# Performance work log

Measured on AMD Instinct MI355X. Metric: run time of the kernel, lower is better.

The kernel has to match this reference:

```python
import jax, jax.numpy as jnp
import numpy as np

N = 2          # batch (upsample scale for sample i is i+1, shapes chosen so no crop occurs)
C = 512        # channels for both branches
TH = TW = 256  # target H,W taken from pts_feats[0]
IMG_SIZES = [128, 64, 32, 16, 8]  # 5-level FPN
BN_EPS = 1e-5


def setup_inputs() -> dict:
    key = jax.random.key(0)
    ks = jax.random.split(key, 24)
    inp = {}
    for l, s in enumerate(IMG_SIZES):
        inp[f'img_feat{l}'] = jax.random.normal(ks[l], (N, C, s, s), jnp.float32)
    inp['pts_feat0'] = jax.random.normal(ks[5], (N, C, TH, TW), jnp.float32)
    # 1x1 conv + BN params (eval-mode BN with running stats)
    inp['img_w'] = jax.random.normal(ks[6], (C, C), jnp.float32) * 0.02
    inp['img_b'] = jax.random.normal(ks[7], (C,), jnp.float32) * 0.02
    inp['img_gamma'] = jnp.ones((C,), jnp.float32)
    inp['img_beta'] = jnp.zeros((C,), jnp.float32)
    inp['img_mean'] = jnp.zeros((C,), jnp.float32)
    inp['img_var'] = jax.random.uniform(ks[8], (C,), jnp.float32, 0.5, 1.5)
    inp['pts_w'] = jax.random.normal(ks[9], (C, C), jnp.float32) * 0.02
    inp['pts_b'] = jax.random.normal(ks[10], (C,), jnp.float32) * 0.02
    inp['pts_gamma'] = jnp.ones((C,), jnp.float32)
    inp['pts_beta'] = jnp.zeros((C,), jnp.float32)
    inp['pts_mean'] = jnp.zeros((C,), jnp.float32)
    inp['pts_var'] = jax.random.uniform(ks[11], (C,), jnp.float32, 0.5, 1.5)
    return inp


def _obtain_mlvl(feats, th, tw):
    # Faithful to original: per-sample loop (scale_factor depends on batch index,
    # so each sample has a different static upsampled shape -> Python loop over N=2).
    n = feats[0].shape[0]
    outs = []
    for i in range(n):
        acc = None
        for lvl, f in enumerate(feats):
            x = f[i]  # [C, h, w]
            if lvl > 0:
                s = i + 1  # nearest upsample by batch-index+1 (as in source)
                x = jnp.repeat(jnp.repeat(x, s, axis=1), s, axis=2)
            dh = th - x.shape[1]
            dw = tw - x.shape[2]
            x = jnp.pad(x, ((0, 0), (dh // 2, dh - dh // 2), (dw // 2, dw - dw // 2)), mode='edge')
            acc = x if acc is None else acc + x
        outs.append(acc)
    return jnp.stack(outs, 0)  # [N, C, th, tw]


def _conv_bn_relu(x, w, b, gamma, beta, mean, var):
    # 1x1 conv == channel contraction, then eval-mode BN, then ReLU
    y = jnp.einsum('nchw,oc->nohw', x, w) + b[None, :, None, None]
    scale = gamma / jnp.sqrt(var + BN_EPS)
    y = (y - mean[None, :, None, None]) * scale[None, :, None, None] + beta[None, :, None, None]
    return jax.nn.relu(y)


def reference(img_feat0, img_feat1, img_feat2, img_feat3, img_feat4, pts_feat0,
              img_w, img_b, img_gamma, img_beta, img_mean, img_var,
              pts_w, pts_b, pts_gamma, pts_beta, pts_mean, pts_var):
    th, tw = pts_feat0.shape[2], pts_feat0.shape[3]
    pts_m = _obtain_mlvl([pts_feat0], th, tw)  # pts_levels=1
    pts_pre = _conv_bn_relu(pts_m, pts_w, pts_b, pts_gamma, pts_beta, pts_mean, pts_var)
    img_m = _obtain_mlvl([img_feat0, img_feat1, img_feat2, img_feat3, img_feat4], th, tw)
    img_pre = _conv_bn_relu(img_m, img_w, img_b, img_gamma, img_beta, img_mean, img_var)
    # dropout is identity in eval mode (deterministic reference)
    return jnp.concatenate((img_pre, pts_pre), axis=1)  # [N, 2C, th, tw]
```

## Files before the change

kernel.cpp:

```cpp
#include <hip/hip_runtime.h>

typedef unsigned short u16;
typedef __attribute__((ext_vector_type(8))) short s8frag;
typedef __attribute__((ext_vector_type(4))) float f32x4;

#define GLOAD16(gp, lp)                                                        \
  __builtin_amdgcn_global_load_lds(                                            \
      (const __attribute__((address_space(1))) void*)(gp),                     \
      (__attribute__((address_space(3))) void*)(lp), 16, 0, 0)

__device__ __forceinline__ u16 f2bf(float x) {
  unsigned int u = __float_as_uint(x);
  unsigned int r = (u + 0x7fffu + ((u >> 16) & 1u)) >> 16;
  return (u16)r;
}

__global__ __launch_bounds__(256) void build_b(
    const float* __restrict__ f0, const float* __restrict__ f1,
    const float* __restrict__ f2, const float* __restrict__ f3,
    const float* __restrict__ f4, const float* __restrict__ pts,
    const float* __restrict__ wi, const float* __restrict__ bi,
    const float* __restrict__ gi, const float* __restrict__ bei,
    const float* __restrict__ mi, const float* __restrict__ vi,
    const float* __restrict__ wp, const float* __restrict__ bp,
    const float* __restrict__ gp, const float* __restrict__ bep,
    const float* __restrict__ mp, const float* __restrict__ vp,
    u16* __restrict__ Bimg, u16* __restrict__ Bpts,
    u16* __restrict__ wA_img, float* __restrict__ bias_i,
    u16* __restrict__ wA_pts, float* __restrict__ bias_p) {
  int t = threadIdx.x;
  int z = blockIdx.z;

  if (z == 32) {
    int base = ((blockIdx.y * 4 + blockIdx.x) * 256 + t) * 2;
#pragma unroll
    for (int e = 0; e < 2; ++e) {
      int gidx = base + e;
      int branch = gidx >> 18;
      int idx = gidx & ((1 << 18) - 1);
      int o = idx >> 9, c = idx & 511;
      const float* w = branch ? wp : wi;
      const float* b = branch ? bp : bi;
      const float* g = branch ? gp : gi;
      const float* be = branch ? bep : bei;
      const float* mn = branch ? mp : mi;
      const float* vr = branch ? vp : vi;
      u16* wo = branch ? wA_pts : wA_img;
      float* bo = branch ? bias_p : bias_i;
      float scale = g[o] * rsqrtf(vr[o] + 1e-5f);
      wo[idx] = f2bf(w[idx] * scale);
      if (c == 0) bo[o] = scale * (b[o] - mn[o]) + be[o];
    }
    return;
  }

  int wblk = blockIdx.x;
  int h = blockIdx.y;
  bool is_img = z < 16;
  int zz = is_img ? z : z - 16;
  int n = zz >> 3;
  int cblk = zz & 7;
  int cbase = cblk * 64;

  if (is_img) {
    __shared__ u16 btile[64][8][8];
    int wl = t & 63, w = wblk * 64 + wl;
    int cg = t >> 6;
    const float* feats[5] = {f0, f1, f2, f3, f4};
    const int S[5] = {128, 64, 32, 16, 8};
    long gbase[5];
#pragma unroll
    for (int l = 0; l < 5; ++l) {
      int sl = S[l];
      int sh = (n == 1 && l > 0) ? 1 : 0;
      int u = sl << sh, pad = (256 - u) >> 1;
      int ih = h - pad; ih = ih < 0 ? 0 : (ih > u - 1 ? u - 1 : ih); ih >>= sh;
      int iw = w - pad; iw = iw < 0 ? 0 : (iw > u - 1 ? u - 1 : iw); iw >>= sh;
      gbase[l] = (long)(n * 512) * sl * sl + ih * sl + iw;
    }
#pragma unroll
    for (int it = 0; it < 2; ++it) {
      int chunk = cg + it * 4;
      int c0 = cbase + chunk * 8;
      u16 pk[8];
#pragma unroll
      for (int j = 0; j < 8; ++j) {
        int c = c0 + j;
        float a_ = 0.f;
#pragma unroll
        for (int l = 0; l < 5; ++l)
          a_ += feats[l][gbase[l] + (long)c * (S[l] * S[l])];
        pk[j] = f2bf(a_);
      }
      *(uint4*)&btile[wl][chunk ^ (wl & 7)][0] = *(const uint4*)pk;
    }
    __syncthreads();
#pragma unroll
    for (int half = 0; half < 2; ++half) {
      int w2 = half * 32 + (t >> 3);
      int kcl = t & 7;
      uint4 v = *(const uint4*)&btile[w2][kcl ^ (w2 & 7)][0];
      long di = ((long)n * 65536 + (long)h * 256 + wblk * 64 + w2) * 512 +
                cbase + kcl * 8;
      *(uint4*)(Bimg + di) = v;
    }
    return;
  }

  __shared__ float tile[64][65];
  int wq = t & 15;
  int cl0 = t >> 4;
#pragma unroll
  for (int j = 0; j < 4; ++j) {
    int cl = cl0 + j * 16;
    int c = cbase + cl;
    float4 v = *(const float4*)&pts[((long)(n * 512 + c) * 256 + h) * 256 +
                                    wblk * 64 + wq * 4];
    tile[cl][wq * 4 + 0] = v.x;
    tile[cl][wq * 4 + 1] = v.y;
    tile[cl][wq * 4 + 2] = v.z;
    tile[cl][wq * 4 + 3] = v.w;
  }
  __syncthreads();

  long hwb = (long)h * 256 + wblk * 64;
#pragma unroll
  for (int half = 0; half < 2; ++half) {
    int c0 = (t & 7) * 8;
    int wl2 = half * 32 + (t >> 3);
    u16 p[8];
#pragma unroll
    for (int j = 0; j < 8; ++j) p[j] = f2bf(tile[c0 + j][wl2]);
    long di = ((long)n * 65536 + hwb + wl2) * 512 + cbase + c0;
    *(uint4*)(Bpts + di) = *(const uint4*)p;
  }
}

__global__ __launch_bounds__(1024, 1) void gemm_fused(
    const u16* __restrict__ Aimg, const u16* __restrict__ Apts,
    const u16* __restrict__ Bimg, const u16* __restrict__ Bpts,
    const float* __restrict__ biasImg, const float* __restrict__ biasPts,
    float* __restrict__ out) {
  int br = blockIdx.z;
  const u16* A = br ? Apts : Aimg;
  const u16* B = br ? Bpts : Bimg;
  const float* bias = br ? biasPts : biasImg;

  int s = blockIdx.x;
  int w = (s & 7) * 128 + (s >> 3);
  int rt = w & 1;
  int ct = w >> 1;
  int n = ct >> 8;
  int colbase = (ct & 255) * 256;
  const u16* Bn = B + ((long)n * 65536) * 512;

  __shared__ u16 As[3][256 * 32];
  __shared__ u16 Bs[3][256 * 32];

  int t = threadIdx.x;
  int wave = t >> 6, lane = t & 63;
  int wr = wave >> 2, wc = wave & 3;
  int lrow = lane & 15;
  int q = lane >> 4;

  f32x4 acc[4][4] = {};

#define STAGE(buf, kt_)                                                       \
  {                                                                           \
    int kk_ = (kt_) * 32;                                                     \
    int row = t >> 2, kp = t & 3;                                             \
    int sw = (row >> 1) & 3;                                                  \
    GLOAD16(A + ((long)(rt * 256 + row) * 512 + kk_ + ((kp ^ sw) * 8)),       \
            &As[buf][(t) * 8]);                                               \
    GLOAD16(Bn + ((long)(colbase + row) * 512 + kk_ + ((kp ^ sw) * 8)),       \
            &Bs[buf][(t) * 8]);                                               \
  }

  STAGE(0, 0);
  STAGE(1, 1);
  asm volatile("s_waitcnt vmcnt(2)" ::: "memory");
  __builtin_amdgcn_s_barrier();

#pragma unroll 1
  for (int kt = 0; kt < 16; ++kt) {
    int cur = kt % 3;
    s8frag a[4], b[4];
#pragma unroll
    for (int m = 0; m < 4; ++m) {
      int r = wr * 64 + m * 16 + lrow;
      a[m] = *(const s8frag*)&As[cur][r * 32 + ((q ^ ((r >> 1) & 3)) * 8)];
    }
#pragma unroll
    for (int nn = 0; nn < 4; ++nn) {
      int r = wc * 64 + nn * 16 + lrow;
      b[nn] = *(const s8frag*)&Bs[cur][r * 32 + ((q ^ ((r >> 1) & 3)) * 8)];
    }
    if (kt < 14) STAGE((kt + 2) % 3, kt + 2);
    __builtin_amdgcn_s_setprio(1);
#pragma unroll
    for (int m = 0; m < 4; ++m)
#pragma unroll
      for (int nn = 0; nn < 4; ++nn)
        acc[m][nn] =
            __builtin_amdgcn_mfma_f32_16x16x32_bf16(b[nn], a[m], acc[m][nn], 0, 0, 0);
    __builtin_amdgcn_s_setprio(0);
    if (kt < 15) {
      if (kt < 14)
        asm volatile("s_waitcnt vmcnt(2)" ::: "memory");
      else
        asm volatile("s_waitcnt vmcnt(0)" ::: "memory");
      __builtin_amdgcn_s_barrier();
    }
  }
#undef STAGE

  long outbase = ((long)n * 1024 + br * 512) * 65536;
#pragma unroll
  for (int m = 0; m < 4; ++m) {
    int o = rt * 256 + wr * 64 + m * 16 + lrow;
    float bv = bias[o];
    long orow = outbase + (long)o * 65536;
#pragma unroll
    for (int nn = 0; nn < 4; ++nn) {
      int hwq = colbase + wc * 64 + nn * 16 + q * 4;
      f32x4 v;
#pragma unroll
      for (int j = 0; j < 4; ++j) {
        float x = acc[m][nn][j] + bv;
        v[j] = x > 0.f ? x : 0.f;
      }
      *(f32x4*)(out + orow + hwq) = v;
    }
  }
}

extern "C" void kernel_launch(void* const* d_in, const int* in_sizes, int n_in,
                              void* d_out, int out_size, void* d_ws,
                              size_t ws_size, hipStream_t stream) {
  (void)in_sizes; (void)n_in; (void)out_size; (void)ws_size;
  const float* f0 = (const float*)d_in[0];
  const float* f1 = (const float*)d_in[1];
  const float* f2 = (const float*)d_in[2];
  const float* f3 = (const float*)d_in[3];
  const float* f4 = (const float*)d_in[4];
  const float* pts = (const float*)d_in[5];
  const float* img_w = (const float*)d_in[6];
  const float* img_b = (const float*)d_in[7];
  const float* img_gamma = (const float*)d_in[8];
  const float* img_beta = (const float*)d_in[9];
  const float* img_mean = (const float*)d_in[10];
  const float* img_var = (const float*)d_in[11];
  const float* pts_w = (const float*)d_in[12];
  const float* pts_b = (const float*)d_in[13];
  const float* pts_gamma = (const float*)d_in[14];
  const float* pts_beta = (const float*)d_in[15];
  const float* pts_mean = (const float*)d_in[16];
  const float* pts_var = (const float*)d_in[17];

  char* ws = (char*)d_ws;
  u16* wA_img = (u16*)ws;
  u16* wA_pts = wA_img + 512 * 512;
  float* bias_img = (float*)(ws + (1u << 20));
  float* bias_pts = bias_img + 512;
  u16* Bimg = (u16*)(ws + (2u << 20));
  u16* Bpts = Bimg + (size_t)2 * 65536 * 512;

  build_b<<<dim3(4, 256, 33), 256, 0, stream>>>(
      f0, f1, f2, f3, f4, pts, img_w, img_b, img_gamma, img_beta, img_mean,
      img_var, pts_w, pts_b, pts_gamma, pts_beta, pts_mean, pts_var, Bimg,
      Bpts, wA_img, bias_img, wA_pts, bias_pts);
  gemm_fused<<<dim3(1024, 1, 2), 1024, 0, stream>>>(
      wA_img, wA_pts, Bimg, Bpts, bias_img, bias_pts, (float*)d_out);
}
```

Baseline: 406.3 us.

## Make GEMM persistent over 8 column tiles with continuous cross-tile prefetch

```diff
diff --git a/kernel.cpp b/kernel.cpp
--- a/kernel.cpp
+++ b/kernel.cpp
@@ -146,13 +146,15 @@
   const u16* B = br ? Bpts : Bimg;
   const float* bias = br ? biasPts : biasImg;
 
-  int s = blockIdx.x;
-  int w = (s & 7) * 128 + (s >> 3);
+  int s0 = blockIdx.x;
+  int w = (s0 & 7) * 16 + (s0 >> 3);
   int rt = w & 1;
-  int ct = w >> 1;
-  int n = ct >> 8;
-  int colbase = (ct & 255) * 256;
+  int grp = w >> 1;
+  int ct0 = grp * 8;
+  int n = ct0 >> 8;
+  int colbase0 = (ct0 & 255) * 256;
   const u16* Bn = B + ((long)n * 65536) * 512;
+  long outbase = ((long)n * 1024 + br * 512) * 65536;
 
   __shared__ u16 As[3][256 * 32];
   __shared__ u16 Bs[3][256 * 32];
@@ -165,25 +167,26 @@
 
   f32x4 acc[4][4] = {};
 
-#define STAGE(buf, kt_)                                                       \
+#define STAGE(s_)                                                             \
   {                                                                           \
-    int kk_ = (kt_) * 32;                                                     \
+    int kk_ = ((s_) & 15) * 32;                                               \
+    int cb_ = colbase0 + ((s_) >> 4) * 256;                                   \
     int row = t >> 2, kp = t & 3;                                             \
     int sw = (row >> 1) & 3;                                                  \
     GLOAD16(A + ((long)(rt * 256 + row) * 512 + kk_ + ((kp ^ sw) * 8)),       \
-            &As[buf][(t) * 8]);                                               \
-    GLOAD16(Bn + ((long)(colbase + row) * 512 + kk_ + ((kp ^ sw) * 8)),       \
-            &Bs[buf][(t) * 8]);                                               \
-  }
-
-  STAGE(0, 0);
-  STAGE(1, 1);
+            &As[(s_) % 3][(t) * 8]);                                          \
+    GLOAD16(Bn + ((long)(cb_ + row) * 512 + kk_ + ((kp ^ sw) * 8)),           \
+            &Bs[(s_) % 3][(t) * 8]);                                          \
+  }
+
+  STAGE(0);
+  STAGE(1);
   asm volatile("s_waitcnt vmcnt(2)" ::: "memory");
   __builtin_amdgcn_s_barrier();
 
 #pragma unroll 1
-  for (int kt = 0; kt < 16; ++kt) {
-    int cur = kt % 3;
+  for (int s = 0; s < 128; ++s) {
+    int cur = s % 3;
     s8frag a[4], b[4];
 #pragma unroll
     for (int m = 0; m < 4; ++m) {
@@ -195,7 +198,7 @@
       int r = wc * 64 + nn * 16 + lrow;
       b[nn] = *(const s8frag*)&Bs[cur][r * 32 + ((q ^ ((r >> 1) & 3)) * 8)];
     }
-    if (kt < 14) STAGE((kt + 2) % 3, kt + 2);
+    if (s < 126) STAGE(s + 2);
     __builtin_amdgcn_s_setprio(1);
 #pragma unroll
     for (int m = 0; m < 4; ++m)
@@ -204,8 +207,31 @@
         acc[m][nn] =
             __builtin_amdgcn_mfma_f32_16x16x32_bf16(b[nn], a[m], acc[m][nn], 0, 0, 0);
     __builtin_amdgcn_s_setprio(0);
-    if (kt < 15) {
-      if (kt < 14)
+
+    if ((s & 15) == 15) {
+      int colbase = colbase0 + (s >> 4) * 256;
+#pragma unroll
+      for (int m = 0; m < 4; ++m) {
+        int o = rt * 256 + wr * 64 + m * 16 + lrow;
+        float bv = bias[o];
+        long orow = outbase + (long)o * 65536;
+#pragma unroll
+        for (int nn = 0; nn < 4; ++nn) {
+          int hwq = colbase + wc * 64 + nn * 16 + q * 4;
+          f32x4 v;
+#pragma unroll
+          for (int j = 0; j < 4; ++j) {
+            float x = acc[m][nn][j] + bv;
+            v[j] = x > 0.f ? x : 0.f;
+          }
+          *(f32x4*)(out + orow + hwq) = v;
+          acc[m][nn] = (f32x4){0.f, 0.f, 0.f, 0.f};
+        }
+      }
+    }
+
+    if (s < 127) {
+      if (s < 126)
         asm volatile("s_waitcnt vmcnt(2)" ::: "memory");
       else
         asm volatile("s_waitcnt vmcnt(0)" ::: "memory");
@@ -213,25 +239,6 @@
     }
   }
 #undef STAGE
-
-  long outbase = ((long)n * 1024 + br * 512) * 65536;
-#pragma unroll
-  for (int m = 0; m < 4; ++m) {
-    int o = rt * 256 + wr * 64 + m * 16 + lrow;
-    float bv = bias[o];
-    long orow = outbase + (long)o * 65536;
-#pragma unroll
-    for (int nn = 0; nn < 4; ++nn) {
-      int hwq = colbase + wc * 64 + nn * 16 + q * 4;
-      f32x4 v;
-#pragma unroll
-      for (int j = 0; j < 4; ++j) {
-        float x = acc[m][nn][j] + bv;
-        v[j] = x > 0.f ? x : 0.f;
-      }
-      *(f32x4*)(out + orow + hwq) = v;
-    }
-  }
 }
 
 extern "C" void kernel_launch(void* const* d_in, const int* in_sizes, int n_in,
@@ -269,6 +276,6 @@
       f0, f1, f2, f3, f4, pts, img_w, img_b, img_gamma, img_beta, img_mean,
       img_var, pts_w, pts_b, pts_gamma, pts_beta, pts_mean, pts_var, Bimg,
       Bpts, wA_img, bias_img, wA_pts, bias_pts);
-  gemm_fused<<<dim3(1024, 1, 2), 1024, 0, stream>>>(
+  gemm_fused<<<dim3(128, 1, 2), 1024, 0, stream>>>(
       wA_img, wA_pts, Bimg, Bpts, bias_img, bias_pts, (float*)d_out);
 }
```

New measurement: 441.6 us. +8.7%, slower.
